# Kernel tuning notes

Hardware: AMD Instinct MI355X
Metric: run time of the kernel (lower is better)

## Reference

```python
import jax, jax.numpy as jnp
import numpy as np

D, H, W, N = 256, 384, 384, 65536


def setup_inputs() -> dict:
    key = jax.random.key(0)
    k1, k2, k3, k4 = jax.random.split(key, 4)
    tokens = jax.random.normal(k1, (N, D), dtype=jnp.float32)
    # unique in-range grid coordinates (duplicates would make scatter-set nondeterministic)
    flat = jax.random.permutation(k2, H * W)[:N]
    coords = jnp.stack([flat // W, flat % W], axis=1).astype(jnp.int32)
    # torch Conv2d default init: U(-b, b), b = 1/sqrt(fan_in), fan_in = (in/groups)*k*k = 9
    bound = 1.0 / np.sqrt(9.0)
    weight = jax.random.uniform(k3, (D, 1, 3, 3), minval=-bound, maxval=bound, dtype=jnp.float32)
    bias = jax.random.uniform(k4, (D,), minval=-bound, maxval=bound, dtype=jnp.float32)
    return {"tokens": tokens, "coords": coords, "weight": weight, "bias": bias,
            "grid_h": H, "grid_w": W}


def reference(tokens, coords, weight, bias, grid_h, grid_w):
    d = tokens.shape[1]
    rows = coords[:, 0]
    cols = coords[:, 1]
    # scatter tokens onto a zero grid: grid[c, r, w] = tokens[n, c]
    grid = jnp.zeros((d, grid_h, grid_w), dtype=tokens.dtype).at[:, rows, cols].set(tokens.T)
    # depthwise 3x3 conv, padding=1 (same)
    conv = jax.lax.conv_general_dilated(
        grid[None], weight,
        window_strides=(1, 1), padding=((1, 1), (1, 1)),
        dimension_numbers=("NCHW", "OIHW", "NCHW"),
        feature_group_count=d,
    ) + bias[None, :, None, None]
    # gather back at the same coordinates -> [N, d]
    return conv[0, :, rows, cols].T
```

## Files before the change

kernel.cpp:

```cpp
#include <hip/hip_runtime.h>

#define DD 256
#define HH 384
#define WW 384
#define NTOK 65536
#define TPB 32
#define TPW 8

__global__ __launch_bounds__(256) void prep_kernel(
    const float* __restrict__ weight, const float* __restrict__ bias,
    float* __restrict__ wT, float* __restrict__ biasf)
{
    int ch = threadIdx.x;
    #pragma unroll
    for (int k = 0; k < 9; ++k)
        wT[k * DD + ch] = weight[ch * 9 + k];
    biasf[ch] = bias[ch];
}

__global__ __launch_bounds__(256) void scatter_pos_kernel(
    const int* __restrict__ coords, int* __restrict__ pos_map)
{
    int n = blockIdx.x * blockDim.x + threadIdx.x;
    if (n < NTOK) {
        int r = coords[2 * n + 0];
        int c = coords[2 * n + 1];
        pos_map[r * WW + c] = n;
    }
}

__global__ __launch_bounds__(256) void conv_gather_kernel(
    const float* __restrict__ tokens,
    const int*   __restrict__ coords,
    const float* __restrict__ wT,
    const float* __restrict__ biasf,
    const int*   __restrict__ pos_map,
    float*       __restrict__ out)
{
    __shared__ float s_out[TPB][DD];

    const int wave = threadIdx.x >> 6;
    const int lane = threadIdx.x & 63;
    const int c0   = lane * 4;
    const int nw   = __builtin_amdgcn_readfirstlane(blockIdx.x * TPB + wave * TPW);

    const float4 bias4 = *(const float4*)(biasf + c0);
    float4 w4[9];
    #pragma unroll
    for (int k = 0; k < 9; ++k)
        w4[k] = *(const float4*)(wT + k * DD + c0);

    int midx[TPW][9];
    #pragma unroll
    for (int i = 0; i < TPW; ++i) {
        const int n = nw + i;
        const int r = coords[2 * n + 0];
        const int c = coords[2 * n + 1];
        #pragma unroll
        for (int dy = 0; dy < 3; ++dy) {
            #pragma unroll
            for (int dx = 0; dx < 3; ++dx) {
                const int k  = dy * 3 + dx;
                const int rr = r + dy - 1;
                const int cc = c + dx - 1;
                const bool in_bounds = (rr >= 0) & (rr < HH) & (cc >= 0) & (cc < WW);
                const int  pidx = in_bounds ? (rr * WW + cc) : 0;
                const int  m    = pos_map[pidx];
                const bool use  = in_bounds & (m >= 0);
                midx[i][k] = use ? m : (n | 0x80000000);
            }
        }
    }

    #pragma unroll
    for (int i = 0; i < TPW; ++i) {
        float4 acc = bias4;
        #pragma unroll
        for (int k = 0; k < 9; ++k) {
            const int   mi  = midx[i][k];
            const int   row = mi & 0x7fffffff;
            const float sel = (mi >= 0) ? 1.0f : 0.0f;
            const float4 t = *(const float4*)(tokens + (size_t)row * DD + c0);
            acc.x += w4[k].x * (sel * t.x);
            acc.y += w4[k].y * (sel * t.y);
            acc.z += w4[k].z * (sel * t.z);
            acc.w += w4[k].w * (sel * t.w);
        }
        *(float4*)&s_out[wave * TPW + i][c0] = acc;
    }
    __syncthreads();

    const int ch = threadIdx.x;
    float* dst = out + (size_t)ch * NTOK + blockIdx.x * TPB;
    #pragma unroll
    for (int j = 0; j < 8; ++j) {
        float4 v;
        v.x = s_out[4 * j + 0][ch];
        v.y = s_out[4 * j + 1][ch];
        v.z = s_out[4 * j + 2][ch];
        v.w = s_out[4 * j + 3][ch];
        *(float4*)(dst + 4 * j) = v;
    }
}

extern "C" void kernel_launch(void* const* d_in, const int* in_sizes, int n_in,
                              void* d_out, int out_size, void* d_ws, size_t ws_size,
                              hipStream_t stream)
{
    const float* tokens = (const float*)d_in[0];
    const int*   coords = (const int*)d_in[1];
    const float* weight = (const float*)d_in[2];
    const float* bias   = (const float*)d_in[3];
    float* out = (float*)d_out;

    char* ws = (char*)d_ws;
    float* wT      = (float*)ws;
    float* biasf   = (float*)(ws + 9216);
    int*   pos_map = (int*)(ws + 16384);

    hipMemsetAsync(pos_map, 0xFF, (size_t)HH * WW * sizeof(int), stream);
    prep_kernel<<<1, 256, 0, stream>>>(weight, bias, wT, biasf);
    scatter_pos_kernel<<<(NTOK + 255) / 256, 256, 0, stream>>>(coords, pos_map);
    conv_gather_kernel<<<NTOK / TPB, 256, 0, stream>>>(tokens, coords, wT, biasf,
                                                       pos_map, out);
}
```

Before: 174.1 us.

## Double-buffer token gathers and enlarge blocks to 64 tokens with 512 threads

Prefetches the nine neighbour token rows for the next token into a register buffer while the current token's accumulation runs, so gather latency overlaps with FMA work. It also doubles tokens per block to 64 with 512 threads, which gives 64 consecutive output floats per channel in the transposed store and halves the number of blocks. The cost is higher register pressure from the two 9-float4 buffers on top of midx, plus 64 KB of shared memory per block, which can lower occupancy.

```diff
diff --git a/kernel.cpp b/kernel.cpp
--- a/kernel.cpp
+++ b/kernel.cpp
@@ -4,7 +4,7 @@
 #define HH 384
 #define WW 384
 #define NTOK 65536
-#define TPB 32
+#define TPB 64
 #define TPW 8
 
 __global__ __launch_bounds__(256) void prep_kernel(
@@ -29,7 +29,7 @@
     }
 }
 
-__global__ __launch_bounds__(256) void conv_gather_kernel(
+__global__ __launch_bounds__(512) void conv_gather_kernel(
     const float* __restrict__ tokens,
     const int*   __restrict__ coords,
     const float* __restrict__ wT,
@@ -72,33 +72,49 @@
         }
     }
 
+    float4 tbuf[2][9];
+    float  sbuf[2][9];
+    #pragma unroll
+    for (int k = 0; k < 9; ++k) {
+        const int mi = midx[0][k];
+        tbuf[0][k] = *(const float4*)(tokens + (size_t)(mi & 0x7fffffff) * DD + c0);
+        sbuf[0][k] = (mi >= 0) ? 1.0f : 0.0f;
+    }
     #pragma unroll
     for (int i = 0; i < TPW; ++i) {
+        const int cur = i & 1;
+        const int nxt = cur ^ 1;
+        if (i + 1 < TPW) {
+            #pragma unroll
+            for (int k = 0; k < 9; ++k) {
+                const int mi = midx[i + 1][k];
+                tbuf[nxt][k] = *(const float4*)(tokens + (size_t)(mi & 0x7fffffff) * DD + c0);
+                sbuf[nxt][k] = (mi >= 0) ? 1.0f : 0.0f;
+            }
+        }
         float4 acc = bias4;
         #pragma unroll
         for (int k = 0; k < 9; ++k) {
-            const int   mi  = midx[i][k];
-            const int   row = mi & 0x7fffffff;
-            const float sel = (mi >= 0) ? 1.0f : 0.0f;
-            const float4 t = *(const float4*)(tokens + (size_t)row * DD + c0);
-            acc.x += w4[k].x * (sel * t.x);
-            acc.y += w4[k].y * (sel * t.y);
-            acc.z += w4[k].z * (sel * t.z);
-            acc.w += w4[k].w * (sel * t.w);
+            const float sel = sbuf[cur][k];
+            acc.x += w4[k].x * (sel * tbuf[cur][k].x);
+            acc.y += w4[k].y * (sel * tbuf[cur][k].y);
+            acc.z += w4[k].z * (sel * tbuf[cur][k].z);
+            acc.w += w4[k].w * (sel * tbuf[cur][k].w);
         }
         *(float4*)&s_out[wave * TPW + i][c0] = acc;
     }
     __syncthreads();
 
-    const int ch = threadIdx.x;
-    float* dst = out + (size_t)ch * NTOK + blockIdx.x * TPB;
+    const int ch   = threadIdx.x & 255;
+    const int half = threadIdx.x >> 8;
+    float* dst = out + (size_t)ch * NTOK + blockIdx.x * TPB + half * 32;
     #pragma unroll
     for (int j = 0; j < 8; ++j) {
         float4 v;
-        v.x = s_out[4 * j + 0][ch];
-        v.y = s_out[4 * j + 1][ch];
-        v.z = s_out[4 * j + 2][ch];
-        v.w = s_out[4 * j + 3][ch];
+        v.x = s_out[half * 32 + 4 * j + 0][ch];
+        v.y = s_out[half * 32 + 4 * j + 1][ch];
+        v.z = s_out[half * 32 + 4 * j + 2][ch];
+        v.w = s_out[half * 32 + 4 * j + 3][ch];
         *(float4*)(dst + 4 * j) = v;
     }
 }
@@ -121,6 +137,6 @@
     hipMemsetAsync(pos_map, 0xFF, (size_t)HH * WW * sizeof(int), stream);
     prep_kernel<<<1, 256, 0, stream>>>(weight, bias, wT, biasf);
     scatter_pos_kernel<<<(NTOK + 255) / 256, 256, 0, stream>>>(coords, pos_map);
-    conv_gather_kernel<<<NTOK / TPB, 256, 0, stream>>>(tokens, coords, wT, biasf,
+    conv_gather_kernel<<<NTOK / TPB, 512, 0, stream>>>(tokens, coords, wT, biasf,
                                                        pos_map, out);
 }
```

Result: slower. 194.9 us (+12.0%).
